# Optimization experiments

Hardware: AMD Instinct MI355X
Metric: run time of the kernel (lower is better)

Reference implementation:

```python
import jax, jax.numpy as jnp
import numpy as np

B, S, E, H = 4, 2048, 1024, 16
D = E // H  # head_dim = 64
SCALE = D ** -0.5
THETA = 10000.0


def _rope_tables(seq_len, head_dim):
    half = head_dim // 2
    inv_freq = 1.0 / (THETA ** (jnp.arange(half, dtype=jnp.float32) / half))
    ang = jnp.arange(seq_len, dtype=jnp.float32)[:, None] * inv_freq[None, :]  # [S, D/2]
    ang = jnp.concatenate([ang, ang], axis=-1)  # [S, D]
    return jnp.cos(ang), jnp.sin(ang)


def setup_inputs() -> dict:
    key = jax.random.key(0)
    kx, kw, ko = jax.random.split(key, 3)
    x = jax.random.normal(kx, (B, S, E), dtype=jnp.float32)
    in_proj_weight = jax.random.normal(kw, (3 * E, E), dtype=jnp.float32) * (E ** -0.5)
    in_proj_bias = jnp.zeros((3 * E,), dtype=jnp.float32)
    out_w = jax.random.normal(ko, (E, E), dtype=jnp.float32) * (E ** -0.5)
    out_b = jnp.zeros((E,), dtype=jnp.float32)
    cos, sin = _rope_tables(S, D)
    return {"x": x, "in_proj_weight": in_proj_weight, "in_proj_bias": in_proj_bias,
            "out_w": out_w, "out_b": out_b, "cos": cos, "sin": sin}


def _rotate_half(t):
    t1, t2 = jnp.split(t, 2, axis=-1)
    return jnp.concatenate([-t2, t1], axis=-1)


def reference(x, in_proj_weight, in_proj_bias, out_w, out_b, cos, sin):
    b, s, e = x.shape
    # fused QKV projection: [b, s, 3E]
    proj = x @ in_proj_weight.T + in_proj_bias
    q, k, v = jnp.split(proj, 3, axis=-1)
    # b s (h d) -> b h s d
    to_heads = lambda t: t.reshape(b, s, H, D).transpose(0, 2, 1, 3)
    q, k, v = to_heads(q), to_heads(k), to_heads(v)
    # RoPE (rotate-half) on q, k; cos/sin: [S, D] broadcast over batch/heads
    c = cos[None, None, :, :]
    sn = sin[None, None, :, :]
    q = q * c + _rotate_half(q) * sn
    k = k * c + _rotate_half(k) * sn
    # SDPA, non-causal, explicit scale = head_dim**-0.5
    scores = jnp.einsum("bhqd,bhkd->bhqk", q, k) * SCALE
    attn = jax.nn.softmax(scores, axis=-1)
    o = jnp.einsum("bhqk,bhkd->bhqd", attn, v)
    # b h s d -> b s (h d)
    o = o.transpose(0, 2, 1, 3).reshape(b, s, e)
    return o @ out_w.T + out_b
```

## Files before the change

### kernel.cpp

```cpp
#include <hip/hip_runtime.h>

#define NB 4
#define NS 2048
#define NE 1024
#define NH 16
#define ND 64
#define KVB 64

typedef unsigned short ushort_t;
typedef __attribute__((ext_vector_type(8))) short bf16x8;
typedef __attribute__((ext_vector_type(4))) float f32x4;

#define KQPRE 0.18033688011112042f

static __device__ __forceinline__ ushort_t f2bf(float f) {
    union { float f; unsigned int u; } v; v.f = f;
    unsigned int r = v.u + 0x7FFF + ((v.u >> 16) & 1);
    return (ushort_t)(r >> 16);
}
static __device__ __forceinline__ float bf2f(ushort_t b) {
    union { unsigned u; float f; } v; v.u = ((unsigned)b) << 16;
    return v.f;
}

static __device__ __forceinline__ unsigned pk_bf16(float lo, float hi) {
    unsigned r;
    asm("v_cvt_pk_bf16_f32 %0, %1, %2" : "=v"(r) : "v"(lo), "v"(hi));
    return r;
}

static __device__ __forceinline__ void gload16(const void* g, void* l) {
    __builtin_amdgcn_global_load_lds(
        (const __attribute__((address_space(1))) void*)g,
        (__attribute__((address_space(3))) void*)l,
        16, 0, 0);
}

__global__ __launch_bounds__(256)
void cvt3_f32_bf16(const float* __restrict__ x,  ushort_t* __restrict__ xb,
                   const float* __restrict__ Wi, ushort_t* __restrict__ Wib,
                   const float* __restrict__ Wo, ushort_t* __restrict__ Wob)
{
    const int blk = blockIdx.x;
    const float* src; ushort_t* dst; int i;
    if (blk < 4096)      { src = x;  dst = xb;  i = blk * 256 + threadIdx.x; }
    else if (blk < 5632) { src = Wi; dst = Wib; i = (blk - 4096) * 256 + threadIdx.x; }
    else                 { src = Wo; dst = Wob; i = (blk - 5632) * 256 + threadIdx.x; }
    const float4 a = ((const float4*)src)[i * 2];
    const float4 b = ((const float4*)src)[i * 2 + 1];
    union { ushort_t us[8]; uint4 v; } pk;
    pk.us[0] = f2bf(a.x); pk.us[1] = f2bf(a.y); pk.us[2] = f2bf(a.z); pk.us[3] = f2bf(a.w);
    pk.us[4] = f2bf(b.x); pk.us[5] = f2bf(b.y); pk.us[6] = f2bf(b.z); pk.us[7] = f2bf(b.w);
    ((uint4*)dst)[i] = pk.v;
}

template<int EPI>
__global__ __launch_bounds__(256)
void gemm_bf16(const ushort_t* __restrict__ A, const ushort_t* __restrict__ W,
               const float* __restrict__ bias, float* __restrict__ C,
               ushort_t* __restrict__ Cb, const float* __restrict__ cosT,
               const float* __restrict__ sinT, int M, int N, int K)
{
    __shared__ ushort_t As[128 * 32];
    __shared__ ushort_t Bs[128 * 32];
    const int tid  = threadIdx.x;
    const int lane = tid & 63;
    const int wid  = tid >> 6;
    const int lr   = lane & 15;
    const int lg   = lane >> 4;

    const int lin   = blockIdx.y * gridDim.x + blockIdx.x;
    const int chunk = (gridDim.x * gridDim.y) >> 3;
    const int lin2  = (lin & 7) * chunk + (lin >> 3);
    const int bx    = lin2 % gridDim.x;
    const int by    = lin2 / gridDim.x;
    const int m0 = by * 128;
    const int n0 = bx * 128;
    const int wr = wid >> 1, wc = wid & 1;

    size_t srcoff[2];
    int ldsoff[2];
#pragma unroll
    for (int p = 0; p < 2; ++p) {
        const int chnk = p * 256 + tid;
        const int row = chnk >> 2;
        const int sp  = chnk & 3;
        const int c   = sp ^ ((row >> 1) & 3);
        srcoff[p] = (size_t)row * K + c * 8;
        ldsoff[p] = (p * 256 + wid * 64) * 8;
    }
    const ushort_t* Ag = A + (size_t)m0 * K;
    const ushort_t* Wg = W + (size_t)n0 * K;

    int offa[4], offb[4];
#pragma unroll
    for (int f = 0; f < 4; ++f) {
        const int ra = wr * 64 + f * 16 + lr;
        offa[f] = ra * 32 + (lg ^ ((ra >> 1) & 3)) * 8;
        const int rb = wc * 64 + f * 16 + lr;
        offb[f] = rb * 32 + (lg ^ ((rb >> 1) & 3)) * 8;
    }

    f32x4 acc[4][4];
#pragma unroll
    for (int i = 0; i < 4; ++i)
#pragma unroll
        for (int j = 0; j < 4; ++j) acc[i][j] = (f32x4){0.f, 0.f, 0.f, 0.f};

    for (int k0 = 0; k0 < K; k0 += 32) {
        __syncthreads();
#pragma unroll
        for (int p = 0; p < 2; ++p) {
            gload16(Ag + srcoff[p] + k0, (ushort_t*)As + ldsoff[p]);
            gload16(Wg + srcoff[p] + k0, (ushort_t*)Bs + ldsoff[p]);
        }
        __syncthreads();
        bf16x8 af[4], bfr[4];
#pragma unroll
        for (int f = 0; f < 4; ++f) {
            af[f]  = *(const bf16x8*)&As[offa[f]];
            bfr[f] = *(const bf16x8*)&Bs[offb[f]];
        }
#pragma unroll
        for (int mf = 0; mf < 4; ++mf)
#pragma unroll
            for (int nf = 0; nf < 4; ++nf)
                acc[mf][nf] = __builtin_amdgcn_mfma_f32_16x16x32_bf16(
                    af[mf], bfr[nf], acc[mf][nf], 0, 0, 0);
    }

    if (EPI == 0) {
#pragma unroll
        for (int nf = 0; nf < 4; ++nf) {
            const int n = n0 + wc * 64 + nf * 16 + lr;
            const float bj = bias[n];
#pragma unroll
            for (int mf = 0; mf < 4; ++mf)
#pragma unroll
                for (int r = 0; r < 4; ++r) {
                    const int m = m0 + wr * 64 + mf * 16 + lg * 4 + r;
                    C[(size_t)m * N + n] = acc[mf][nf][r] + bj;
                }
        }
    } else {
        const int tt = n0 >> 10;
        float bj[4]; int hh[4];
#pragma unroll
        for (int nf = 0; nf < 4; ++nf) {
            const int n = n0 + wc * 64 + nf * 16 + lr;
            bj[nf] = bias[n];
            hh[nf] = (n >> 6) & (NH - 1);
        }
#pragma unroll
        for (int mf = 0; mf < 4; ++mf)
#pragma unroll
            for (int r = 0; r < 4; ++r) {
                const int m = m0 + wr * 64 + mf * 16 + lg * 4 + r;
                const int b = m >> 11;
                const int s = m & (NS - 1);
                float v[4];
#pragma unroll
                for (int nf = 0; nf < 4; ++nf) v[nf] = acc[mf][nf][r] + bj[nf];
                if (tt < 2) {
#pragma unroll
                    for (int p = 0; p < 2; ++p) {
                        const int d = p * 16 + lr;
                        const float c  = cosT[s * ND + d];
                        const float sn = sinT[s * ND + d];
                        const float lo = v[p] * c - v[p + 2] * sn;
                        const float hi = v[p + 2] * c + v[p] * sn;
                        v[p] = lo; v[p + 2] = hi;
                    }
                    if (tt == 0) {
#pragma unroll
                        for (int nf = 0; nf < 4; ++nf) v[nf] *= KQPRE;
                    }
                }
#pragma unroll
                for (int nf = 0; nf < 4; ++nf)
                    Cb[((size_t)((tt * NB + b) * NH + hh[nf]) * NS + s) * ND
                       + nf * 16 + lr] = f2bf(v[nf]);
            }
    }
}

__global__ __launch_bounds__(256)
void attn_kernel(const ushort_t* __restrict__ qkvb, ushort_t* __restrict__ obuf)
{
    __shared__ ushort_t Ks[64 * 72];
    __shared__ ushort_t Vs[64 * 64];
    __shared__ ushort_t Ps[128 * 72];

    const int tid  = threadIdx.x;
    const int lane = tid & 63;
    const int wid  = tid >> 6;
    const int lr   = lane & 15;
    const int lg   = lane >> 4;

    const int orig = blockIdx.x;
    const int wg   = (orig & 7) * 128 + (orig >> 3);
    const int bh   = wg >> 4;
    const int b = bh >> 4, h = bh & (NH - 1);
    const int q0 = (wg & 15) * 128;

    const ushort_t* qbase = qkvb + ((size_t)((0 * NB + b) * NH + h)) * (NS * ND);
    const ushort_t* kbase = qkvb + ((size_t)((1 * NB + b) * NH + h)) * (NS * ND);
    const ushort_t* vbase = qkvb + ((size_t)((2 * NB + b) * NH + h)) * (NS * ND);

    bf16x8 onesf;
#pragma unroll
    for (int j = 0; j < 8; ++j) onesf[j] = (short)0x3F80;

    bf16x8 qf[2][2];
#pragma unroll
    for (int st = 0; st < 2; ++st)
#pragma unroll
        for (int kh = 0; kh < 2; ++kh)
            qf[st][kh] = *(const bf16x8*)(qbase + (size_t)(q0 + wid * 32 + st * 16 + lr) * ND
                                          + kh * 32 + lg * 8);

    const int sc = tid & 7;
    const int sr0 = tid >> 3;

    uint4 krg[2], vrg[2];
#pragma unroll
    for (int it = 0; it < 2; ++it) {
        const int r = sr0 + it * 32;
        krg[it] = *(const uint4*)(kbase + r * ND + sc * 8);
        vrg[it] = *(const uint4*)(vbase + r * ND + sc * 8);
    }

    f32x4 acc_o[2][4];
    f32x4 acc_l[2];
#pragma unroll
    for (int st = 0; st < 2; ++st) {
        acc_l[st] = (f32x4){0.f, 0.f, 0.f, 0.f};
#pragma unroll
        for (int dk = 0; dk < 4; ++dk) acc_o[st][dk] = (f32x4){0.f, 0.f, 0.f, 0.f};
    }

    for (int kt = 0; kt < NS; kt += KVB) {
        __syncthreads();
#pragma unroll
        for (int it = 0; it < 2; ++it) {
            const int r = sr0 + it * 32;
            *(uint4*)&Ks[r * 72 + sc * 8] = krg[it];
            union { uint4 v; ushort_t us[8]; } pu;
            pu.v = vrg[it];
#pragma unroll
            for (int j = 0; j < 8; ++j) {
                const int sw = (j ^ sc) << 4;
                Vs[(sc * 8 + j) * 64 + ((((r * 2) ^ sw)) >> 1)] = pu.us[j];
            }
        }
        __syncthreads();
        if (kt + KVB < NS) {
#pragma unroll
            for (int it = 0; it < 2; ++it) {
                const int r = kt + KVB + sr0 + it * 32;
                krg[it] = *(const uint4*)(kbase + (size_t)r * ND + sc * 8);
                vrg[it] = *(const uint4*)(vbase + (size_t)r * ND + sc * 8);
            }
        }

        f32x4 s[2][4];
#pragma unroll
        for (int st = 0; st < 2; ++st)
#pragma unroll
            for (int kvf = 0; kvf < 4; ++kvf) s[st][kvf] = (f32x4){0.f, 0.f, 0.f, 0.f};
        __builtin_amdgcn_s_setprio(1);
#pragma unroll
        for (int kh = 0; kh < 2; ++kh)
#pragma unroll
            for (int kvf = 0; kvf < 4; ++kvf) {
                const bf16x8 kf = *(const bf16x8*)&Ks[(kvf * 16 + lr) * 72 + kh * 32 + lg * 8];
                s[0][kvf] = __builtin_amdgcn_mfma_f32_16x16x32_bf16(kf, qf[0][kh], s[0][kvf], 0, 0, 0);
                s[1][kvf] = __builtin_amdgcn_mfma_f32_16x16x32_bf16(kf, qf[1][kh], s[1][kvf], 0, 0, 0);
            }
        __builtin_amdgcn_s_setprio(0);

#pragma unroll
        for (int st = 0; st < 2; ++st) {
            const int prow = (wid * 32 + st * 16 + lr) * 72;
#pragma unroll
            for (int kvf = 0; kvf < 4; ++kvf) {
                const float p0 = __builtin_amdgcn_exp2f(s[st][kvf][0]);
                const float p1 = __builtin_amdgcn_exp2f(s[st][kvf][1]);
                const float p2 = __builtin_amdgcn_exp2f(s[st][kvf][2]);
                const float p3 = __builtin_amdgcn_exp2f(s[st][kvf][3]);
                const unsigned w01 = pk_bf16(p0, p1);
                const unsigned w23 = pk_bf16(p2, p3);
                *(uint2*)&Ps[prow + kvf * 16 + lg * 4] = make_uint2(w01, w23);
            }
        }
        asm volatile("s_waitcnt lgkmcnt(0)" ::: "memory");
        __builtin_amdgcn_sched_barrier(0);

        __builtin_amdgcn_s_setprio(1);
#pragma unroll
        for (int kh = 0; kh < 2; ++kh) {
            const bf16x8 pf0 = *(const bf16x8*)&Ps[(wid * 32 + 0  + lr) * 72 + kh * 32 + lg * 8];
            const bf16x8 pf1 = *(const bf16x8*)&Ps[(wid * 32 + 16 + lr) * 72 + kh * 32 + lg * 8];
            acc_l[0] = __builtin_amdgcn_mfma_f32_16x16x32_bf16(pf0, onesf, acc_l[0], 0, 0, 0);
            acc_l[1] = __builtin_amdgcn_mfma_f32_16x16x32_bf16(pf1, onesf, acc_l[1], 0, 0, 0);
#pragma unroll
            for (int dk = 0; dk < 4; ++dk) {
                const int d = dk * 16 + lr;
                const int sw = ((d & 7) ^ ((d >> 3) & 7)) << 4;
                const bf16x8 vf = *(const bf16x8*)&Vs[d * 64 + (((kh * 64 + lg * 16) ^ sw) >> 1)];
                acc_o[0][dk] = __builtin_amdgcn_mfma_f32_16x16x32_bf16(pf0, vf, acc_o[0][dk], 0, 0, 0);
                acc_o[1][dk] = __builtin_amdgcn_mfma_f32_16x16x32_bf16(pf1, vf, acc_o[1][dk], 0, 0, 0);
            }
        }
        __builtin_amdgcn_s_setprio(0);
    }

#pragma unroll
    for (int st = 0; st < 2; ++st) {
        float invq[4];
#pragma unroll
        for (int reg = 0; reg < 4; ++reg)
            invq[reg] = 1.0f / acc_l[st][reg];
#pragma unroll
        for (int dk = 0; dk < 4; ++dk)
#pragma unroll
            for (int reg = 0; reg < 4; ++reg) {
                const int q = q0 + wid * 32 + st * 16 + lg * 4 + reg;
                const int d = dk * 16 + lr;
                obuf[((size_t)(b * NS + q)) * NE + h * ND + d] =
                    f2bf(acc_o[st][dk][reg] * invq[reg]);
            }
    }
}

extern "C" void kernel_launch(void* const* d_in, const int* in_sizes, int n_in,
                              void* d_out, int out_size, void* d_ws, size_t ws_size,
                              hipStream_t stream)
{
    const float* x    = (const float*)d_in[0];
    const float* Win  = (const float*)d_in[1];
    const float* bin  = (const float*)d_in[2];
    const float* Wout = (const float*)d_in[3];
    const float* bout = (const float*)d_in[4];
    const float* cosT = (const float*)d_in[5];
    const float* sinT = (const float*)d_in[6];
    float* out  = (float*)d_out;

    ushort_t* qkvb  = (ushort_t*)d_ws;
    ushort_t* obufb = qkvb + (size_t)3 * NB * NH * NS * ND;
    ushort_t* xb    = obufb + (size_t)NB * NS * NE;
    ushort_t* Wib   = xb + (size_t)NB * NS * NE;
    ushort_t* Wob   = Wib + (size_t)3 * NE * NE;

    cvt3_f32_bf16<<<6144, 256, 0, stream>>>(x, xb, Win, Wib, Wout, Wob);

    gemm_bf16<1><<<dim3(3 * NE / 128, NB * NS / 128), 256, 0, stream>>>(
        xb, Wib, bin, nullptr, qkvb, cosT, sinT, NB * NS, 3 * NE, NE);
    attn_kernel<<<dim3(NB * NH * (NS / 128)), 256, 0, stream>>>(qkvb, obufb);
    gemm_bf16<0><<<dim3(NE / 128, NB * NS / 128), 256, 0, stream>>>(
        obufb, Wob, bout, out, nullptr, nullptr, nullptr, NB * NS, NE, NE);
}
```

Measured before the change: 231.6 us.

## Replace QKV projection GEMM with 256x256-tile double-buffered direct-to-LDS kernel

Adds a dedicated QKV GEMM kernel with 256x256 output tiles, 512 threads, a K-step of 64 and two LDS buffers filled by async global-to-LDS loads. Loads for tile t+2 are issued while MFMAs run on the current tile, with setprio and swizzled LDS layout. The kernel keeps the existing fused bias, RoPE and Q-scaling epilogue. The aim is to raise MFMA utilization and data reuse over the old 128x128 tile kernel, at the cost of large LDS use and a 384-block grid that may leave a partial wave.

Measured after the change: 231.2 us, median of 2. No clear change (-0.2%).

```diff
diff --git a/kernel.cpp b/kernel.cpp
--- a/kernel.cpp
+++ b/kernel.cpp
@@ -54,6 +54,158 @@
     ((uint4*)dst)[i] = pk.v;
 }
 
+__global__ __launch_bounds__(512, 2)
+void gemm1_256(const ushort_t* __restrict__ A, const ushort_t* __restrict__ W,
+               const float* __restrict__ bias, ushort_t* __restrict__ Cb,
+               const float* __restrict__ cosT, const float* __restrict__ sinT)
+{
+    const int M = NB * NS, N = 3 * NE, K = NE;
+    const int NK = K / 64;
+    __shared__ ushort_t As[2][256 * 64];
+    __shared__ ushort_t Bs[2][256 * 64];
+
+    const int tid  = threadIdx.x;
+    const int lane = tid & 63;
+    const int wid  = tid >> 6;
+    const int lr   = lane & 15;
+    const int lg   = lane >> 4;
+    const int wr   = wid >> 2;
+    const int wc   = wid & 3;
+
+    const int orig = blockIdx.x;
+    const int wg   = (orig & 7) * 48 + (orig >> 3);
+    const int bx   = wg % 12;
+    const int by   = wg / 12;
+    const int m0 = by * 256, n0 = bx * 256;
+    (void)M;
+
+    size_t srcA[4], srcB[4];
+    int dstoff[4];
+#pragma unroll
+    for (int p = 0; p < 4; ++p) {
+        const int g   = p * 512 + tid;
+        const int row = g >> 3;
+        const int cl  = (g & 7) ^ (row & 7);
+        srcA[p] = (size_t)(m0 + row) * K + cl * 8;
+        srcB[p] = (size_t)(n0 + row) * K + cl * 8;
+        dstoff[p] = (p * 512 + wid * 64) * 8;
+    }
+
+    const int x7  = lr & 7;
+    const int pc0 = ((0 + lg) ^ x7) * 8;
+    const int pc1 = ((4 + lg) ^ x7) * 8;
+    int offa[8], offb[4];
+#pragma unroll
+    for (int mf = 0; mf < 8; ++mf) offa[mf] = (wr * 128 + mf * 16 + lr) * 64;
+#pragma unroll
+    for (int nf = 0; nf < 4; ++nf) offb[nf] = (wc * 64 + nf * 16 + lr) * 64;
+
+    f32x4 acc[8][4];
+#pragma unroll
+    for (int i = 0; i < 8; ++i)
+#pragma unroll
+        for (int j = 0; j < 4; ++j) acc[i][j] = (f32x4){0.f, 0.f, 0.f, 0.f};
+
+#pragma unroll
+    for (int p = 0; p < 4; ++p) {
+        gload16(A + srcA[p], (ushort_t*)As[0] + dstoff[p]);
+        gload16(W + srcB[p], (ushort_t*)Bs[0] + dstoff[p]);
+    }
+#pragma unroll
+    for (int p = 0; p < 4; ++p) {
+        gload16(A + srcA[p] + 64, (ushort_t*)As[1] + dstoff[p]);
+        gload16(W + srcB[p] + 64, (ushort_t*)Bs[1] + dstoff[p]);
+    }
+    asm volatile("s_waitcnt vmcnt(8)" ::: "memory");
+    __builtin_amdgcn_s_barrier();
+    __builtin_amdgcn_sched_barrier(0);
+
+    int cur = 0;
+    for (int t = 0; t < NK; ++t) {
+        bf16x8 af[8], bfv[4];
+#pragma unroll
+        for (int mf = 0; mf < 8; ++mf) af[mf] = *(const bf16x8*)&As[cur][offa[mf] + pc0];
+#pragma unroll
+        for (int nf = 0; nf < 4; ++nf) bfv[nf] = *(const bf16x8*)&Bs[cur][offb[nf] + pc0];
+        __builtin_amdgcn_s_setprio(1);
+#pragma unroll
+        for (int mf = 0; mf < 8; ++mf)
+#pragma unroll
+            for (int nf = 0; nf < 4; ++nf)
+                acc[mf][nf] = __builtin_amdgcn_mfma_f32_16x16x32_bf16(
+                    af[mf], bfv[nf], acc[mf][nf], 0, 0, 0);
+        __builtin_amdgcn_s_setprio(0);
+#pragma unroll
+        for (int mf = 0; mf < 8; ++mf) af[mf] = *(const bf16x8*)&As[cur][offa[mf] + pc1];
+#pragma unroll
+        for (int nf = 0; nf < 4; ++nf) bfv[nf] = *(const bf16x8*)&Bs[cur][offb[nf] + pc1];
+        asm volatile("s_waitcnt lgkmcnt(0)" ::: "memory");
+        __builtin_amdgcn_sched_barrier(0);
+        __builtin_amdgcn_s_barrier();
+        __builtin_amdgcn_sched_barrier(0);
+        if (t + 2 < NK) {
+            const int koff = (t + 2) * 64;
+#pragma unroll
+            for (int p = 0; p < 4; ++p) {
+                gload16(A + srcA[p] + koff, (ushort_t*)As[cur] + dstoff[p]);
+                gload16(W + srcB[p] + koff, (ushort_t*)Bs[cur] + dstoff[p]);
+            }
+        }
+        __builtin_amdgcn_s_setprio(1);
+#pragma unroll
+        for (int mf = 0; mf < 8; ++mf)
+#pragma unroll
+            for (int nf = 0; nf < 4; ++nf)
+                acc[mf][nf] = __builtin_amdgcn_mfma_f32_16x16x32_bf16(
+                    af[mf], bfv[nf], acc[mf][nf], 0, 0, 0);
+        __builtin_amdgcn_s_setprio(0);
+        if (t + 1 < NK) {
+            if (t + 2 < NK) asm volatile("s_waitcnt vmcnt(8)" ::: "memory");
+            else            asm volatile("s_waitcnt vmcnt(0)" ::: "memory");
+            __builtin_amdgcn_s_barrier();
+            __builtin_amdgcn_sched_barrier(0);
+        }
+        cur ^= 1;
+    }
+
+    const int tt = n0 >> 10;
+    const int nbase = n0 + wc * 64;
+    const int h = (nbase >> 6) & (NH - 1);
+    float bj[4];
+#pragma unroll
+    for (int nf = 0; nf < 4; ++nf) bj[nf] = bias[nbase + nf * 16 + lr];
+#pragma unroll
+    for (int mf = 0; mf < 8; ++mf)
+#pragma unroll
+        for (int r = 0; r < 4; ++r) {
+            const int m = m0 + wr * 128 + mf * 16 + lg * 4 + r;
+            const int b = m >> 11;
+            const int s = m & (NS - 1);
+            float v[4];
+#pragma unroll
+            for (int nf = 0; nf < 4; ++nf) v[nf] = acc[mf][nf][r] + bj[nf];
+            if (tt < 2) {
+#pragma unroll
+                for (int p = 0; p < 2; ++p) {
+                    const int d = p * 16 + lr;
+                    const float c  = cosT[s * ND + d];
+                    const float sn = sinT[s * ND + d];
+                    const float lo = v[p] * c - v[p + 2] * sn;
+                    const float hi = v[p + 2] * c + v[p] * sn;
+                    v[p] = lo; v[p + 2] = hi;
+                }
+                if (tt == 0) {
+#pragma unroll
+                    for (int nf = 0; nf < 4; ++nf) v[nf] *= KQPRE;
+                }
+            }
+#pragma unroll
+            for (int nf = 0; nf < 4; ++nf)
+                Cb[((size_t)((tt * NB + b) * NH + h) * NS + s) * ND
+                   + nf * 16 + lr] = f2bf(v[nf]);
+        }
+}
+
 template<int EPI>
 __global__ __launch_bounds__(256)
 void gemm_bf16(const ushort_t* __restrict__ A, const ushort_t* __restrict__ W,
@@ -354,8 +506,7 @@
 
     cvt3_f32_bf16<<<6144, 256, 0, stream>>>(x, xb, Win, Wib, Wout, Wob);
 
-    gemm_bf16<1><<<dim3(3 * NE / 128, NB * NS / 128), 256, 0, stream>>>(
-        xb, Wib, bin, nullptr, qkvb, cosT, sinT, NB * NS, 3 * NE, NE);
+    gemm1_256<<<384, 512, 0, stream>>>(xb, Wib, bin, qkvb, cosT, sinT);
     attn_kernel<<<dim3(NB * NH * (NS / 128)), 256, 0, stream>>>(qkvb, obufb);
     gemm_bf16<0><<<dim3(NE / 128, NB * NS / 128), 256, 0, stream>>>(
         obufb, Wob, bout, out, nullptr, nullptr, nullptr, NB * NS, NE, NE);
```
